# Kernel optimization log

Measured on AMD Instinct MI355X. Metric: run time of the kernel, lower is better.

The kernel has to match this reference:

```python
import jax, jax.numpy as jnp
import numpy as np

BUCKET_SIZE = 64
N_HASHES = 8
SELF_MASK_VAL = -1e5
EPS = 1e-6


def look_one_back(x):
    # concat each block with the previous block (wrap-around), along block-inner axis
    prev = jnp.roll(x, 1, axis=1)
    return jnp.concatenate([x, prev], axis=2)


def setup_inputs() -> dict:
    key = jax.random.key(0)
    k1, k2, k3 = jax.random.split(key, 3)
    B, S, D = 8, 4096, 64
    n_buckets = S // BUCKET_SIZE  # 64
    qk = jax.random.normal(k1, (B, S, D), dtype=jnp.float32)
    v = jax.random.normal(k2, (B, S, D), dtype=jnp.float32)
    rotations = jax.random.normal(k3, (1, D, N_HASHES, n_buckets // 2), dtype=jnp.float32)
    return {"qk": qk, "v": v, "rotations": rotations}


def reference(qk, v, rotations):
    B, S, D = qk.shape
    n_buckets = S // BUCKET_SIZE
    n_bins = n_buckets

    # --- hash_vectors ---
    rot = jnp.broadcast_to(rotations, (B, D, N_HASHES, n_buckets // 2))
    rotated = jnp.einsum('btf,bfhi->bhti', qk, rot)            # [B,H,S,nb/2]
    rotated = jnp.concatenate([rotated, -rotated], axis=-1)    # [B,H,S,nb]
    buckets = jnp.argmax(rotated, axis=-1)                     # [B,H,S]
    offsets = (jnp.arange(N_HASHES) * n_buckets)[None, :, None]
    buckets = (buckets + offsets).reshape(B, N_HASHES * S)     # [B,H*S]

    # --- sort tokens by (bucket, position) ---
    ticker = jnp.arange(N_HASHES * S)[None, :]
    buckets_and_t = S * buckets + (ticker % S)
    sticker = jnp.argsort(buckets_and_t, axis=-1)              # stable sort
    undo_sort = jnp.argsort(sticker, axis=-1)
    st = sticker % S                                           # original positions

    sqk = jnp.take_along_axis(qk, st[..., None], axis=1)       # [B,H*S,D]
    sv = jnp.take_along_axis(v, st[..., None], axis=1)

    n_blocks = N_HASHES * n_bins
    bq_t = st.reshape(B, n_blocks, -1)                         # [B,nb,bs]
    bqk = sqk.reshape(B, n_blocks, -1, D)
    bv = sv.reshape(B, n_blocks, -1, D)

    bq = bqk
    # make_unit_length
    bk = bqk * jax.lax.rsqrt(jnp.sum(bqk * bqk, axis=-1, keepdims=True) + EPS)
    bk = look_one_back(bk)                                     # [B,nb,2bs,D]
    bv = look_one_back(bv)
    bkv_t = look_one_back(bq_t[..., None])[..., 0]             # [B,nb,2bs]

    dots = jnp.einsum('bhie,bhje->bhij', bq, bk) * (D ** -0.5)  # [B,nb,bs,2bs]

    # self-mask (as written in source: keep dots where positions equal, -1e5 elsewhere)
    self_mask = bq_t[:, :, :, None] == bkv_t[:, :, None, :]
    dots = jnp.where(self_mask, dots, SELF_MASK_VAL)

    dots_lse = jax.scipy.special.logsumexp(dots, axis=-1, keepdims=True)
    probs = jnp.exp(dots - dots_lse)
    bo = jnp.einsum('buij,buje->buie', probs, bv)              # [B,nb,bs,D]

    so = bo.reshape(B, N_HASHES * S, D)
    slogits = dots_lse.reshape(B, N_HASHES * S)

    # unsort
    o = jnp.take_along_axis(so, undo_sort[..., None], axis=1)
    logits = jnp.take_along_axis(slogits, undo_sort, axis=1)

    # combine over hash rounds
    o = o.reshape(B, N_HASHES, S, D)
    logits = logits.reshape(B, N_HASHES, S, 1)
    w = jnp.exp(logits - jax.scipy.special.logsumexp(logits, axis=1, keepdims=True))
    out = jnp.sum(o * w, axis=1)                               # [B,S,D]
    return out, buckets
```

## Files before the change

kernel.cpp:

```cpp
#include <hip/hip_runtime.h>

#define BB 8
#define SS 4096
#define DD 64
#define NH 8
#define NBKT 64
#define OUT_V_ELEMS (BB*SS*DD)

__global__ __launch_bounds__(256) void lsh_hash_kernel(
    const float* __restrict__ qk,
    const float* __restrict__ v,
    const float* __restrict__ rot,
    float* __restrict__ out)
{
    __shared__ float rot_s[64 * 128];
    __shared__ float qk_s[64 * 68];

    const int tid = threadIdx.x;
    const int blk = blockIdx.x;
    const int b   = blk >> 7;
    const int r   = blk & 127;
    const int hh  = r >> 6;
    const int tc  = r & 63;
    const int t0  = tc * 64;

    {
        const float4* v4 = (const float4*)v;
        float4*       o4 = (float4*)out;
        const int base = blk * 512 + tid;
        o4[base]       = v4[base];
        o4[base + 256] = v4[base + 256];
    }

    {
        const float4* rg = (const float4*)rot;
#pragma unroll
        for (int k = 0; k < 8; ++k) {
            const int p = tid + k * 256;
            const int f = p >> 5, q = p & 31;
            const float4 rr = rg[f * 64 + hh * 32 + q];
            *(float4*)&rot_s[f * 128 + q * 4] = rr;
        }
    }
    {
        const float4* qg = (const float4*)qk;
#pragma unroll
        for (int k = 0; k < 4; ++k) {
            const int p  = tid + k * 256;
            const int tt = p >> 4, fq = p & 15;
            const float4 g = qg[(b * SS + t0 + tt) * 16 + fq];
            qk_s[(fq * 4 + 0) * 68 + tt] = g.x;
            qk_s[(fq * 4 + 1) * 68 + tt] = g.y;
            qk_s[(fq * 4 + 2) * 68 + tt] = g.z;
            qk_s[(fq * 4 + 3) * 68 + tt] = g.w;
        }
    }
    __syncthreads();

    const int tg    = tid & 15;
    const int hg    = tid >> 4;
    const int hl    = hg >> 2;
    const int ibase = (hg & 3) * 8;
    const int hglob = hh * 4 + hl;

    float acc[4][8];
#pragma unroll
    for (int a = 0; a < 4; ++a)
#pragma unroll
        for (int c = 0; c < 8; ++c) acc[a][c] = 0.0f;

#pragma unroll 4
    for (int f = 0; f < 64; ++f) {
        const float4 q4 = *(const float4*)&qk_s[f * 68 + tg * 4];
        const float4 r0 = *(const float4*)&rot_s[f * 128 + hg * 8];
        const float4 r1 = *(const float4*)&rot_s[f * 128 + hg * 8 + 4];
        const float qa[4] = {q4.x, q4.y, q4.z, q4.w};
        const float rr[8] = {r0.x, r0.y, r0.z, r0.w, r1.x, r1.y, r1.z, r1.w};
#pragma unroll
        for (int a = 0; a < 4; ++a)
#pragma unroll
            for (int c = 0; c < 8; ++c)
                acc[a][c] = fmaf(qa[a], rr[c], acc[a][c]);
    }

    float bq[4];
#pragma unroll
    for (int a = 0; a < 4; ++a) {
        float pv = acc[a][0]; int pi = ibase;
        float nv = -acc[a][0]; int ni = ibase;
#pragma unroll
        for (int c = 1; c < 8; ++c) {
            const float x = acc[a][c];
            if (x  > pv) { pv = x;  pi = ibase + c; }
            if (-x > nv) { nv = -x; ni = ibase + c; }
        }
#pragma unroll
        for (int m = 16; m <= 32; m <<= 1) {
            const float opv = __shfl_xor(pv, m, 64);
            const int   opi = __shfl_xor(pi, m, 64);
            const float onv = __shfl_xor(nv, m, 64);
            const int   oni = __shfl_xor(ni, m, 64);
            if (opv > pv || (opv == pv && opi < pi)) { pv = opv; pi = opi; }
            if (onv > nv || (onv == nv && oni < ni)) { nv = onv; ni = oni; }
        }
        const int idx = (pv >= nv) ? pi : (ni + 32);
        bq[a] = (float)(idx + hglob * NBKT);
    }

    if ((hg & 3) == 0) {
        float4 w; w.x = bq[0]; w.y = bq[1]; w.z = bq[2]; w.w = bq[3];
        *(float4*)&out[OUT_V_ELEMS + b * (NH * SS) + hglob * SS + t0 + tg * 4] = w;
    }
}

extern "C" void kernel_launch(void* const* d_in, const int* in_sizes, int n_in,
                              void* d_out, int out_size, void* d_ws, size_t ws_size,
                              hipStream_t stream) {
    const float* qk  = (const float*)d_in[0];
    const float* v   = (const float*)d_in[1];
    const float* rot = (const float*)d_in[2];
    float* out = (float*)d_out;
    hipLaunchKernelGGL(lsh_hash_kernel, dim3(1024), dim3(256), 0, stream,
                       qk, v, rot, out);
}
```

Before: 23.70 us.

## Read rotations as wave-uniform scalar loads and give each lane one token

```diff
diff --git a/kernel.cpp b/kernel.cpp
--- a/kernel.cpp
+++ b/kernel.cpp
@@ -13,14 +13,13 @@
     const float* __restrict__ rot,
     float* __restrict__ out)
 {
-    __shared__ float rot_s[64 * 128];
-    __shared__ float qk_s[64 * 68];
+    __shared__ float qk_s[64 * 64];
 
     const int tid = threadIdx.x;
     const int blk = blockIdx.x;
     const int b   = blk >> 7;
     const int r   = blk & 127;
-    const int hh  = r >> 6;
+    const int hq  = r >> 6;
     const int tc  = r & 63;
     const int t0  = tc * 64;
 
@@ -33,84 +32,55 @@
     }
 
     {
-        const float4* rg = (const float4*)rot;
-#pragma unroll
-        for (int k = 0; k < 8; ++k) {
-            const int p = tid + k * 256;
-            const int f = p >> 5, q = p & 31;
-            const float4 rr = rg[f * 64 + hh * 32 + q];
-            *(float4*)&rot_s[f * 128 + q * 4] = rr;
-        }
-    }
-    {
         const float4* qg = (const float4*)qk;
 #pragma unroll
         for (int k = 0; k < 4; ++k) {
-            const int p  = tid + k * 256;
-            const int tt = p >> 4, fq = p & 15;
-            const float4 g = qg[(b * SS + t0 + tt) * 16 + fq];
-            qk_s[(fq * 4 + 0) * 68 + tt] = g.x;
-            qk_s[(fq * 4 + 1) * 68 + tt] = g.y;
-            qk_s[(fq * 4 + 2) * 68 + tt] = g.z;
-            qk_s[(fq * 4 + 3) * 68 + tt] = g.w;
+            const int p   = tid + k * 256;
+            const int tok = p >> 4, g = p & 15;
+            const float4 x = qg[(b * SS + t0 + tok) * 16 + g];
+            *(float4*)&qk_s[tok * 64 + ((g ^ (tok & 15)) << 2)] = x;
         }
     }
     __syncthreads();
 
-    const int tg    = tid & 15;
-    const int hg    = tid >> 4;
-    const int hl    = hg >> 2;
-    const int ibase = (hg & 3) * 8;
-    const int hglob = hh * 4 + hl;
+    const int lane = tid & 63;
+    const int h    = hq * 4 + (tid >> 6);
+    const int h_u  = __builtin_amdgcn_readfirstlane(h);
+    const float* __restrict__ rot_h = rot + h_u * 32;
 
-    float acc[4][8];
+    float acc[32];
 #pragma unroll
-    for (int a = 0; a < 4; ++a)
+    for (int i = 0; i < 32; ++i) acc[i] = 0.0f;
+
+    const int lrow = lane * 64;
+    const int lsw  = lane & 15;
+
 #pragma unroll
-        for (int c = 0; c < 8; ++c) acc[a][c] = 0.0f;
-
-#pragma unroll 4
-    for (int f = 0; f < 64; ++f) {
-        const float4 q4 = *(const float4*)&qk_s[f * 68 + tg * 4];
-        const float4 r0 = *(const float4*)&rot_s[f * 128 + hg * 8];
-        const float4 r1 = *(const float4*)&rot_s[f * 128 + hg * 8 + 4];
+    for (int fg = 0; fg < 16; ++fg) {
+        const float4 q4 = *(const float4*)&qk_s[lrow + ((fg ^ lsw) << 2)];
         const float qa[4] = {q4.x, q4.y, q4.z, q4.w};
-        const float rr[8] = {r0.x, r0.y, r0.z, r0.w, r1.x, r1.y, r1.z, r1.w};
 #pragma unroll
-        for (int a = 0; a < 4; ++a)
+        for (int j = 0; j < 4; ++j) {
+            const float* __restrict__ rp = rot_h + (fg * 4 + j) * (NH * 32);
+            float rr[32];
 #pragma unroll
-            for (int c = 0; c < 8; ++c)
-                acc[a][c] = fmaf(qa[a], rr[c], acc[a][c]);
+            for (int i = 0; i < 32; ++i) rr[i] = rp[i];
+            const float qf = qa[j];
+#pragma unroll
+            for (int i = 0; i < 32; ++i)
+                acc[i] = fmaf(qf, rr[i], acc[i]);
+        }
     }
 
-    float bq[4];
+    float pv = acc[0]; int pi = 0;
+    float nv = -acc[0]; int ni = 0;
 #pragma unroll
-    for (int a = 0; a < 4; ++a) {
-        float pv = acc[a][0]; int pi = ibase;
-        float nv = -acc[a][0]; int ni = ibase;
-#pragma unroll
-        for (int c = 1; c < 8; ++c) {
-            const float x = acc[a][c];
-            if (x  > pv) { pv = x;  pi = ibase + c; }
-            if (-x > nv) { nv = -x; ni = ibase + c; }
-        }
-#pragma unroll
-        for (int m = 16; m <= 32; m <<= 1) {
-            const float opv = __shfl_xor(pv, m, 64);
-            const int   opi = __shfl_xor(pi, m, 64);
-            const float onv = __shfl_xor(nv, m, 64);
-            const int   oni = __shfl_xor(ni, m, 64);
-            if (opv > pv || (opv == pv && opi < pi)) { pv = opv; pi = opi; }
-            if (onv > nv || (onv == nv && oni < ni)) { nv = onv; ni = oni; }
-        }
-        const int idx = (pv >= nv) ? pi : (ni + 32);
-        bq[a] = (float)(idx + hglob * NBKT);
+    for (int i = 1; i < 32; ++i) {
+        if (acc[i]  > pv) { pv = acc[i];  pi = i; }
+        if (-acc[i] > nv) { nv = -acc[i]; ni = i; }
     }
-
-    if ((hg & 3) == 0) {
-        float4 w; w.x = bq[0]; w.y = bq[1]; w.z = bq[2]; w.w = bq[3];
-        *(float4*)&out[OUT_V_ELEMS + b * (NH * SS) + hglob * SS + t0 + tg * 4] = w;
-    }
+    const int idx = (pv >= nv) ? pi : (ni + 32);
+    out[OUT_V_ELEMS + b * (NH * SS) + h * SS + t0 + lane] = (float)(idx + h * NBKT);
 }
 
 extern "C" void kernel_launch(void* const* d_in, const int* in_sizes, int n_in,
```

Measured after the change: 26.29 us. 10.9% more time.
